# Kernel optimization log

Hardware: AMD Instinct MI355X
Metric: run time of the kernel (lower is better)

The kernel has to match this reference:

```python
import jax, jax.numpy as jnp
import numpy as np

B, C, H, P = 8, 3, 384, 16
DIM, DEPTH, HEADS, MLP = 768, 8, 12, 3072
NP_ = (H // P) ** 2  # 576 patches
PD = C * P * P       # patch_dim = 768
EPS = 1e-5


def _ln(x, g, b):
    m = jnp.mean(x, axis=-1, keepdims=True)
    v = jnp.mean((x - m) ** 2, axis=-1, keepdims=True)
    return (x - m) / jnp.sqrt(v + EPS) * g + b


def setup_inputs() -> dict:
    key = jax.random.key(0)
    ks = jax.random.split(key, 16)
    s = 0.02
    return {
        "img": jax.random.normal(ks[0], (B, C, H, H), jnp.float32),
        "pos_embedding": jax.random.normal(ks[1], (1, NP_ + 1, DIM), jnp.float32),
        "cls_token": jax.random.normal(ks[2], (1, 1, DIM), jnp.float32),
        "patch_w": jax.random.normal(ks[3], (PD, DIM), jnp.float32) * s,
        "patch_b": jnp.zeros((DIM,), jnp.float32),
        "ln1_g": jnp.ones((DEPTH, DIM), jnp.float32),
        "ln1_b": jnp.zeros((DEPTH, DIM), jnp.float32),
        "qkv_w": jax.random.normal(ks[4], (DEPTH, DIM, 3 * DIM), jnp.float32) * s,
        "out_w": jax.random.normal(ks[5], (DEPTH, DIM, DIM), jnp.float32) * s,
        "out_b": jnp.zeros((DEPTH, DIM), jnp.float32),
        "ln2_g": jnp.ones((DEPTH, DIM), jnp.float32),
        "ln2_b": jnp.zeros((DEPTH, DIM), jnp.float32),
        "ff1_w": jax.random.normal(ks[6], (DEPTH, DIM, MLP), jnp.float32) * s,
        "ff1_b": jnp.zeros((DEPTH, MLP), jnp.float32),
        "ff2_w": jax.random.normal(ks[7], (DEPTH, MLP, DIM), jnp.float32) * s,
        "ff2_b": jnp.zeros((DEPTH, DIM), jnp.float32),
    }


def reference(img, pos_embedding, cls_token, patch_w, patch_b,
              ln1_g, ln1_b, qkv_w, out_w, out_b,
              ln2_g, ln2_b, ff1_w, ff1_b, ff2_w, ff2_b):
    b = img.shape[0]
    hp = H // P
    # b c (h p1) (w p2) -> b (h w) (p1 p2 c)
    x = img.reshape(b, C, hp, P, hp, P).transpose(0, 2, 4, 3, 5, 1).reshape(b, hp * hp, P * P * C)
    x = x @ patch_w + patch_b
    x = jnp.concatenate([jnp.broadcast_to(cls_token, (b, 1, DIM)), x], axis=1)
    x = x + pos_embedding[:, : x.shape[1]]

    def layer(xc, p):
        g1, b1, wqkv, wo, bo, g2, b2, w1, bf1, w2, bf2 = p
        y = _ln(xc, g1, b1)
        qkv = y @ wqkv
        q, k, v = jnp.split(qkv, 3, axis=-1)
        sp = lambda a: a.reshape(b, -1, HEADS, DIM // HEADS).transpose(0, 2, 1, 3)
        q, k, v = sp(q), sp(k), sp(v)
        # NOTE: original code never applies the 1/sqrt(d) scale -- faithful.
        dots = jnp.einsum('bhid,bhjd->bhij', q, k)
        attn = jax.nn.softmax(dots, axis=-1)
        o = jnp.einsum('bhij,bhjd->bhid', attn, v).transpose(0, 2, 1, 3).reshape(b, -1, DIM)
        xc = xc + (o @ wo + bo)
        y = _ln(xc, g2, b2)
        xc = xc + (jax.nn.gelu(y @ w1 + bf1, approximate=False) @ w2 + bf2)
        return xc, None

    x, _ = jax.lax.scan(layer, x, (ln1_g, ln1_b, qkv_w, out_w, out_b,
                                   ln2_g, ln2_b, ff1_w, ff1_b, ff2_w, ff2_b))
    return x[:, 1:, :]
```

## Files before the change

kernel.cpp:

```cpp
#include <hip/hip_runtime.h>
#include <hip/hip_bf16.h>
#include <math.h>

#define BB 8
#define CC 3
#define HH 384
#define PP 16
#define HP 24
#define NP 576
#define PD 768
#define DIM 768
#define DEPTH 8
#define HEADS 12
#define DH 64
#define MLP 3072
#define SS 577
#define BS (BB*SS)
#define MPAD 4736
#define LN_EPS 1e-5f
#define NKT 10
#define QW (3*DIM)

typedef __attribute__((ext_vector_type(8))) short s8v;
typedef __attribute__((ext_vector_type(4))) float f4v;

__device__ __forceinline__ float bf2f(unsigned short s) {
    union { unsigned u; float f; } x;
    x.u = ((unsigned)s) << 16;
    return x.f;
}
__device__ __forceinline__ unsigned short f2bfu(float f) {
    __hip_bfloat16 h = __float2bfloat16(f);
    return *reinterpret_cast<unsigned short*>(&h);
}

__device__ __forceinline__ void async16(void* lds, const void* g) {
    __builtin_amdgcn_global_load_lds(
        (const __attribute__((address_space(1))) void*)(uintptr_t)g,
        (__attribute__((address_space(3))) void*)(unsigned)(uintptr_t)lds,
        16, 0, 0);
}

__global__ __launch_bounds__(256) void patchify_k(const float* __restrict__ img,
                                                  unsigned short* __restrict__ xp) {
    int idx = blockIdx.x * 256 + threadIdx.x;
    const int total = BB * NP * PD;
    if (idx >= total) return;
    int b = idx / (NP * PD);
    int r = idx % (NP * PD);
    int n = r / PD;
    int j = r % PD;
    int c  = j % CC;
    int t  = j / CC;
    int p2 = t % PP;
    int p1 = t / PP;
    int hh = n / HP;
    int ww = n % HP;
    int row = hh * PP + p1;
    int col = ww * PP + p2;
    xp[idx] = f2bfu(img[(((size_t)b * CC + c) * HH + row) * HH + col]);
}

__global__ __launch_bounds__(256) void convT_k(const float* __restrict__ W,
                                               unsigned short* __restrict__ Wt,
                                               int K, int N) {
    __shared__ float t[32][33];
    int tx = threadIdx.x & 31, ty = threadIdx.x >> 5;
    int n0 = blockIdx.x * 32, k0 = blockIdx.y * 32;
#pragma unroll
    for (int i = 0; i < 32; i += 8)
        t[ty + i][tx] = W[(size_t)(k0 + ty + i) * N + n0 + tx];
    __syncthreads();
#pragma unroll
    for (int i = 0; i < 32; i += 8)
        Wt[(size_t)(n0 + ty + i) * K + k0 + tx] = f2bfu(t[tx][ty + i]);
}

__global__ __launch_bounds__(256) void convT4_k(const float* __restrict__ s0,
                                                const float* __restrict__ s1,
                                                const float* __restrict__ s2,
                                                const float* __restrict__ s3,
                                                unsigned short* __restrict__ d0,
                                                unsigned short* __restrict__ d1,
                                                unsigned short* __restrict__ d2,
                                                unsigned short* __restrict__ d3) {
    __shared__ float t[32][33];
    int bid = blockIdx.x;
    const float* S; unsigned short* D; int K, N, lt;
    if (bid < 1728)      { S = s0; D = d0; K = 768;  N = 2304; lt = bid; }
    else if (bid < 2304) { S = s1; D = d1; K = 768;  N = 768;  lt = bid - 1728; }
    else if (bid < 4608) { S = s2; D = d2; K = 768;  N = 3072; lt = bid - 2304; }
    else                 { S = s3; D = d3; K = 3072; N = 768;  lt = bid - 4608; }
    int ntn = N >> 5;
    int n0 = (lt % ntn) * 32, k0 = (lt / ntn) * 32;
    int tx = threadIdx.x & 31, ty = threadIdx.x >> 5;
#pragma unroll
    for (int i = 0; i < 32; i += 8)
        t[ty + i][tx] = S[(size_t)(k0 + ty + i) * N + n0 + tx];
    __syncthreads();
#pragma unroll
    for (int i = 0; i < 32; i += 8)
        D[(size_t)(n0 + ty + i) * K + k0 + tx] = f2bfu(t[tx][ty + i]);
}

__global__ __launch_bounds__(256) void build_x_k(const float* __restrict__ pe,
                                                 const float* __restrict__ cls,
                                                 const float* __restrict__ pos,
                                                 float* __restrict__ x) {
    int idx = blockIdx.x * 256 + threadIdx.x;
    const int total = BB * SS * DIM;
    if (idx >= total) return;
    int b = idx / (SS * DIM);
    int r = idx % (SS * DIM);
    int i = r / DIM;
    int d = r % DIM;
    float p = pos[i * DIM + d];
    float v = (i == 0) ? cls[d] : pe[((size_t)b * NP + (i - 1)) * DIM + d];
    x[idx] = v + p;
}

template <int NPART>
__global__ __launch_bounds__(256) void ln_k(const float* __restrict__ x,
                                            const float* __restrict__ P,
                                            const float* __restrict__ g,
                                            const float* __restrict__ bt,
                                            unsigned short* __restrict__ y,
                                            float* __restrict__ xout) {
    __shared__ float sm[8];
    int row = blockIdx.x, tid = threadIdx.x;
    const float* xr = x + (size_t)row * DIM;
    float v0 = xr[tid], v1 = xr[tid + 256], v2 = xr[tid + 512];
    if (NPART == 2) {
        const float* p0 = P + (size_t)row * DIM;
        const float* p1 = P + (size_t)(BS + row) * DIM;
        v0 += p0[tid]       + p1[tid];
        v1 += p0[tid + 256] + p1[tid + 256];
        v2 += p0[tid + 512] + p1[tid + 512];
        float* xo = xout + (size_t)row * DIM;
        xo[tid] = v0; xo[tid + 256] = v1; xo[tid + 512] = v2;
    }
    float s = v0 + v1 + v2;
    for (int o = 32; o; o >>= 1) s += __shfl_xor(s, o);
    if ((tid & 63) == 0) sm[tid >> 6] = s;
    __syncthreads();
    float mean = (sm[0] + sm[1] + sm[2] + sm[3]) * (1.f / 768.f);
    float q0 = v0 - mean, q1 = v1 - mean, q2 = v2 - mean;
    float s2 = q0 * q0 + q1 * q1 + q2 * q2;
    for (int o = 32; o; o >>= 1) s2 += __shfl_xor(s2, o);
    if ((tid & 63) == 0) sm[4 + (tid >> 6)] = s2;
    __syncthreads();
    float var = (sm[4] + sm[5] + sm[6] + sm[7]) * (1.f / 768.f);
    float rstd = rsqrtf(var + LN_EPS);
    unsigned short* yr = y + (size_t)row * DIM;
    yr[tid]       = f2bfu(q0 * rstd * g[tid]       + bt[tid]);
    yr[tid + 256] = f2bfu(q1 * rstd * g[tid + 256] + bt[tid + 256]);
    yr[tid + 512] = f2bfu(q2 * rstd * g[tid + 512] + bt[tid + 512]);
}

template <int OP, int SPLIT>
__global__ __launch_bounds__(256) void mgemm_k(const unsigned short* __restrict__ A,
                                               const unsigned short* __restrict__ Bt,
                                               const float* __restrict__ bias,
                                               void* __restrict__ Cv,
                                               int M, int N, int K) {
    __shared__ unsigned short Al[2][128 * 32];
    __shared__ unsigned short Bl[2][128 * 32];
    int tid = threadIdx.x;
    int wv = tid >> 6, lane = tid & 63;
    int quad = lane >> 4, l16 = lane & 15;
    int m0 = blockIdx.y * 128, n0 = blockIdx.x * 128;
    int wm = (wv >> 1) * 64, wn = (wv & 1) * 64;
    int rg = lane >> 2;
    int kc = (lane & 3) * 8;

    const int Ks = K / SPLIT;
    const int kbase = blockIdx.z * Ks;
    const int T = Ks / 32;

    f4v acc[4][4];
    const f4v zero = {0.f, 0.f, 0.f, 0.f};
#pragma unroll
    for (int i = 0; i < 4; ++i)
#pragma unroll
        for (int j = 0; j < 4; ++j) acc[i][j] = zero;

    auto stage = [&](int t, int bufi) {
#pragma unroll
        for (int gg = 0; gg < 2; ++gg) {
            int g = wv + gg * 4;
            const unsigned short* ga =
                A + (size_t)(m0 + g * 16 + rg) * K + kbase + t * 32 + kc;
            async16(&Al[bufi][g * 512], ga);
            const unsigned short* gb =
                Bt + (size_t)(n0 + g * 16 + rg) * K + kbase + t * 32 + kc;
            async16(&Bl[bufi][g * 512], gb);
        }
    };

    stage(0, 0);
    __syncthreads();

    for (int t = 0; t < T; ++t) {
        int cur = t & 1;
        if (t + 1 < T) stage(t + 1, cur ^ 1);

        s8v af[4], bfr[4];
#pragma unroll
        for (int i = 0; i < 4; ++i)
            af[i] = *reinterpret_cast<const s8v*>(&Al[cur][(wm + i * 16 + l16) * 32 + quad * 8]);
#pragma unroll
        for (int j = 0; j < 4; ++j)
            bfr[j] = *reinterpret_cast<const s8v*>(&Bl[cur][(wn + j * 16 + l16) * 32 + quad * 8]);
#pragma unroll
        for (int i = 0; i < 4; ++i)
#pragma unroll
            for (int j = 0; j < 4; ++j)
                acc[i][j] = __builtin_amdgcn_mfma_f32_16x16x32_bf16(af[i], bfr[j], acc[i][j], 0, 0, 0);

        if (t + 1 < T) __syncthreads();
    }

#pragma unroll
    for (int j = 0; j < 4; ++j) {
        int col = n0 + wn + j * 16 + l16;
        float bj = bias ? bias[col] : 0.f;
        if (SPLIT > 1 && blockIdx.z != 0) bj = 0.f;
#pragma unroll
        for (int i = 0; i < 4; ++i) {
#pragma unroll
            for (int r = 0; r < 4; ++r) {
                int row = m0 + wm + i * 16 + quad * 4 + r;
                if (row >= M) continue;
                float v = acc[i][j][r] + bj;
                size_t idx = (size_t)row * N + col;
                if (OP == 0) {
                    ((unsigned short*)Cv)[idx] = f2bfu(v);
                } else if (OP == 1) {
                    v = 0.5f * v * (1.f + erff(v * 0.70710678118654752f));
                    ((unsigned short*)Cv)[idx] = f2bfu(v);
                } else if (OP == 2) {
                    float* C = (float*)Cv;
                    if (SPLIT > 1) atomicAdd(&C[idx], v);
                    else C[idx] += v;
                } else if (OP == 3) {
                    ((float*)Cv)[idx] = v;
                } else {
                    float* C = (float*)Cv + (size_t)blockIdx.z * ((size_t)M * N);
                    C[idx] = v;
                }
            }
        }
    }
}

__global__ __launch_bounds__(256) void mattn_k(const unsigned short* __restrict__ qkv,
                                               unsigned short* __restrict__ o) {
    __shared__ unsigned short Kl[64 * 72];
    __shared__ unsigned short Vt[64 * 72];
    __shared__ unsigned short Pw[4][16 * 72];

    int tid = threadIdx.x;
    int w = tid >> 6, lane = tid & 63, quad = lane >> 4, l16 = lane & 15;
    int bh = blockIdx.x;
    int b = bh / HEADS, h = bh % HEADS;
    int q0 = blockIdx.y * 64;

    int qq = q0 + w * 16 + l16;
    if (qq > SS - 1) qq = SS - 1;
    const unsigned short* qp = qkv + (size_t)(b * SS + qq) * QW + h * DH + quad * 8;
    s8v aq0 = *reinterpret_cast<const s8v*>(qp);
    s8v aq1 = *reinterpret_cast<const s8v*>(qp + 32);

    float m[4], l[4];
    f4v O[4];
    const f4v zero = {0.f, 0.f, 0.f, 0.f};
#pragma unroll
    for (int r = 0; r < 4; ++r) { m[r] = -INFINITY; l[r] = 0.f; }
#pragma unroll
    for (int dg = 0; dg < 4; ++dg) O[dg] = zero;

    for (int t = 0; t < NKT; ++t) {
        int k0 = t * 64;
        __syncthreads();
#pragma unroll
        for (int rr = 0; rr < 2; ++rr) {
            int cid = tid + rr * 256;
            int row = cid >> 3, cb = (cid & 7) * 8;
            s8v kv = *reinterpret_cast<const s8v*>(
                qkv + (size_t)(b * SS + k0 + row) * QW + DIM + h * DH + cb);
            *reinterpret_cast<s8v*>(&Kl[row * 72 + cb]) = kv;
        }
        {
            int kb = (tid & 15) * 4, db = (tid >> 4) * 4;
            const unsigned short* vb = qkv + (size_t)(b * SS + k0 + kb) * QW + 2 * DIM + h * DH + db;
            ushort4 r0 = *reinterpret_cast<const ushort4*>(vb);
            ushort4 r1 = *reinterpret_cast<const ushort4*>(vb + QW);
            ushort4 r2 = *reinterpret_cast<const ushort4*>(vb + 2 * QW);
            ushort4 r3 = *reinterpret_cast<const ushort4*>(vb + 3 * QW);
            ushort4 w0 = {r0.x, r1.x, r2.x, r3.x};
            ushort4 w1 = {r0.y, r1.y, r2.y, r3.y};
            ushort4 w2 = {r0.z, r1.z, r2.z, r3.z};
            ushort4 w3 = {r0.w, r1.w, r2.w, r3.w};
            *reinterpret_cast<ushort4*>(&Vt[(db + 0) * 72 + kb]) = w0;
            *reinterpret_cast<ushort4*>(&Vt[(db + 1) * 72 + kb]) = w1;
            *reinterpret_cast<ushort4*>(&Vt[(db + 2) * 72 + kb]) = w2;
            *reinterpret_cast<ushort4*>(&Vt[(db + 3) * 72 + kb]) = w3;
        }
        __syncthreads();

        f4v s[4];
#pragma unroll
        for (int kk = 0; kk < 4; ++kk) {
            const unsigned short* kp = &Kl[(kk * 16 + l16) * 72 + quad * 8];
            s8v b0 = *reinterpret_cast<const s8v*>(kp);
            s8v b1 = *reinterpret_cast<const s8v*>(kp + 32);
            f4v z = zero;
            z = __builtin_amdgcn_mfma_f32_16x16x32_bf16(aq0, b0, z, 0, 0, 0);
            z = __builtin_amdgcn_mfma_f32_16x16x32_bf16(aq1, b1, z, 0, 0, 0);
            s[kk] = z;
        }
        int kvalid = SS - k0;
        if (kvalid < 64) {
#pragma unroll
            for (int kk = 0; kk < 4; ++kk)
                if (kk * 16 + l16 >= kvalid) {
                    f4v mk = {-1e30f, -1e30f, -1e30f, -1e30f};
                    s[kk] = mk;
                }
        }
        float alpha[4];
#pragma unroll
        for (int r = 0; r < 4; ++r) {
            float mx = fmaxf(fmaxf(s[0][r], s[1][r]), fmaxf(s[2][r], s[3][r]));
#pragma unroll
            for (int off = 1; off < 16; off <<= 1) mx = fmaxf(mx, __shfl_xor(mx, off));
            float mn = fmaxf(m[r], mx);
            alpha[r] = __expf(m[r] - mn);
            m[r] = mn;
            float ps = 0.f;
#pragma unroll
            for (int kk = 0; kk < 4; ++kk) {
                float p = __expf(s[kk][r] - mn);
                ps += p;
                Pw[w][(quad * 4 + r) * 72 + kk * 16 + l16] = f2bfu(p);
            }
#pragma unroll
            for (int off = 1; off < 16; off <<= 1) ps += __shfl_xor(ps, off);
            l[r] = l[r] * alpha[r] + ps;
        }
#pragma unroll
        for (int dg = 0; dg < 4; ++dg)
#pragma unroll
            for (int r = 0; r < 4; ++r) O[dg][r] *= alpha[r];

        s8v ap0 = *reinterpret_cast<const s8v*>(&Pw[w][l16 * 72 + quad * 8]);
        s8v ap1 = *reinterpret_cast<const s8v*>(&Pw[w][l16 * 72 + 32 + quad * 8]);
#pragma unroll
        for (int dg = 0; dg < 4; ++dg) {
            const unsigned short* vp = &Vt[(dg * 16 + l16) * 72 + quad * 8];
            s8v bv0 = *reinterpret_cast<const s8v*>(vp);
            s8v bv1 = *reinterpret_cast<const s8v*>(vp + 32);
            O[dg] = __builtin_amdgcn_mfma_f32_16x16x32_bf16(ap0, bv0, O[dg], 0, 0, 0);
            O[dg] = __builtin_amdgcn_mfma_f32_16x16x32_bf16(ap1, bv1, O[dg], 0, 0, 0);
        }
    }

#pragma unroll
    for (int r = 0; r < 4; ++r) {
        int q = q0 + w * 16 + quad * 4 + r;
        if (q >= SS) continue;
        float inv = 1.f / l[r];
        unsigned short* op = o + (size_t)(b * SS + q) * DIM + h * DH + l16;
#pragma unroll
        for (int dg = 0; dg < 4; ++dg)
            op[dg * 16] = f2bfu(O[dg][r] * inv);
    }
}

template <int NPART>
__global__ __launch_bounds__(256) void copy_out_k(const float* __restrict__ x,
                                                  const float* __restrict__ P,
                                                  float* __restrict__ out) {
    int idx = blockIdx.x * 256 + threadIdx.x;
    const int total = BB * NP * DIM;
    if (idx >= total) return;
    int b = idx / (NP * DIM);
    int r = idx % (NP * DIM);
    int n = r / DIM;
    int d = r % DIM;
    size_t row = (size_t)b * SS + 1 + n;
    float v = x[row * DIM + d];
    if (NPART == 2)
        v += P[row * DIM + d] + P[(size_t)BS * DIM + row * DIM + d];
    out[idx] = v;
}

extern "C" void kernel_launch(void* const* d_in, const int* in_sizes, int n_in,
                              void* d_out, int out_size, void* d_ws, size_t ws_size,
                              hipStream_t stream) {
    const float* img     = (const float*)d_in[0];
    const float* pos     = (const float*)d_in[1];
    const float* cls     = (const float*)d_in[2];
    const float* patch_w = (const float*)d_in[3];
    const float* patch_b = (const float*)d_in[4];
    const float* ln1_g   = (const float*)d_in[5];
    const float* ln1_b   = (const float*)d_in[6];
    const float* qkv_w   = (const float*)d_in[7];
    const float* out_w   = (const float*)d_in[8];
    const float* out_b   = (const float*)d_in[9];
    const float* ln2_g   = (const float*)d_in[10];
    const float* ln2_b   = (const float*)d_in[11];
    const float* ff1_w   = (const float*)d_in[12];
    const float* ff1_b   = (const float*)d_in[13];
    const float* ff2_w   = (const float*)d_in[14];
    const float* ff2_b   = (const float*)d_in[15];
    float* out = (float*)d_out;

    char* base = (char*)d_ws;
    float* x = (float*)base;                          base += (size_t)BS * DIM * 4;
    unsigned short* y_bf   = (unsigned short*)base;   base += (size_t)MPAD * DIM * 2;
    unsigned short* t1_bf  = (unsigned short*)base;   base += (size_t)MPAD * DIM * 2;
    unsigned short* qkv_bf = (unsigned short*)base;   base += (size_t)MPAD * 3 * DIM * 2;
    unsigned short* hid_bf = (unsigned short*)base;   base += (size_t)MPAD * MLP * 2;
    unsigned short* xp_bf  = (unsigned short*)base;   base += (size_t)BB * NP * PD * 2;
    unsigned short* wq_t = (unsigned short*)base;     base += (size_t)(3 * DIM) * DIM * 2;
    unsigned short* wo_t = (unsigned short*)base;     base += (size_t)DIM * DIM * 2;
    unsigned short* w1_t = (unsigned short*)base;     base += (size_t)MLP * DIM * 2;
    unsigned short* w2_t = (unsigned short*)base;     base += (size_t)DIM * MLP * 2;
    float* part = (float*)base;                       base += (size_t)2 * BS * DIM * 4;
    float* pe_f32 = (float*)hid_bf;

    const int threads = 256;
    const int mblk = (BS + 127) / 128;

    patchify_k<<<(BB * NP * PD + 255) / 256, threads, 0, stream>>>(img, xp_bf);
    convT_k<<<dim3(DIM / 32, PD / 32), threads, 0, stream>>>(patch_w, wq_t, PD, DIM);
    mgemm_k<3, 1><<<dim3(DIM / 128, (BB * NP) / 128), threads, 0, stream>>>(
        xp_bf, wq_t, patch_b, pe_f32, BB * NP, DIM, PD);
    build_x_k<<<(BB * SS * DIM + 255) / 256, threads, 0, stream>>>(pe_f32, cls, pos, x);

    for (int l = 0; l < DEPTH; ++l) {
        if (l == 0)
            ln_k<0><<<BS, threads, 0, stream>>>(x, nullptr, ln1_g, ln1_b, y_bf, nullptr);
        else
            ln_k<2><<<BS, threads, 0, stream>>>(x, part, ln1_g + l * DIM, ln1_b + l * DIM,
                                                y_bf, x);
        convT4_k<<<6912, threads, 0, stream>>>(
            qkv_w + (size_t)l * DIM * 3 * DIM,
            out_w + (size_t)l * DIM * DIM,
            ff1_w + (size_t)l * DIM * MLP,
            ff2_w + (size_t)l * MLP * DIM,
            wq_t, wo_t, w1_t, w2_t);
        mgemm_k<0, 1><<<dim3(3 * DIM / 128, mblk), threads, 0, stream>>>(
            y_bf, wq_t, nullptr, qkv_bf, BS, 3 * DIM, DIM);
        mattn_k<<<dim3(BB * HEADS, NKT), threads, 0, stream>>>(qkv_bf, t1_bf);
        mgemm_k<4, 2><<<dim3(DIM / 128, mblk, 2), threads, 0, stream>>>(
            t1_bf, wo_t, out_b + l * DIM, part, BS, DIM, DIM);
        ln_k<2><<<BS, threads, 0, stream>>>(x, part, ln2_g + l * DIM, ln2_b + l * DIM,
                                            y_bf, x);
        mgemm_k<1, 1><<<dim3(MLP / 128, mblk), threads, 0, stream>>>(
            y_bf, w1_t, ff1_b + l * MLP, hid_bf, BS, MLP, DIM);
        mgemm_k<4, 2><<<dim3(DIM / 128, mblk, 2), threads, 0, stream>>>(
            hid_bf, w2_t, ff2_b + l * DIM, part, BS, DIM, MLP);
    }

    copy_out_k<2><<<(BB * NP * DIM + 255) / 256, threads, 0, stream>>>(x, part, out);
}
```

Baseline: 2.019 ms.

## Triple-buffer GEMM LDS staging with XOR swizzle and setprio around MFMA

Moves the bf16 MFMA GEMM from double to triple LDS buffering. Loads are issued two tiles ahead and gated with explicit vmcnt waits plus a single barrier per iteration, so global-load latency can overlap compute. It also XOR-swizzles the 16-byte k-chunk position on both the async store and the fragment read to reduce LDS bank conflicts, and raises wave priority during the MFMA block. This costs more LDS per block, which may lower occupancy, and the hand-counted vmcnt(4) ties correctness to the number of loads per stage.

```diff
diff --git a/kernel.cpp b/kernel.cpp
--- a/kernel.cpp
+++ b/kernel.cpp
@@ -163,15 +163,16 @@
                                                const float* __restrict__ bias,
                                                void* __restrict__ Cv,
                                                int M, int N, int K) {
-    __shared__ unsigned short Al[2][128 * 32];
-    __shared__ unsigned short Bl[2][128 * 32];
+    __shared__ unsigned short Al[3][128 * 32];
+    __shared__ unsigned short Bl[3][128 * 32];
     int tid = threadIdx.x;
     int wv = tid >> 6, lane = tid & 63;
     int quad = lane >> 4, l16 = lane & 15;
     int m0 = blockIdx.y * 128, n0 = blockIdx.x * 128;
     int wm = (wv >> 1) * 64, wn = (wv & 1) * 64;
     int rg = lane >> 2;
-    int kc = (lane & 3) * 8;
+    int kc = (((lane & 3) ^ (rg & 3)) * 8);
+    int rslot = ((quad ^ (l16 & 3)) * 8);
 
     const int Ks = K / SPLIT;
     const int kbase = blockIdx.z * Ks;
@@ -197,28 +198,40 @@
         }
     };
 
-    stage(0, 0);
-    __syncthreads();
-
-    for (int t = 0; t < T; ++t) {
-        int cur = t & 1;
-        if (t + 1 < T) stage(t + 1, cur ^ 1);
-
+    auto compute = [&](int cur) {
         s8v af[4], bfr[4];
 #pragma unroll
         for (int i = 0; i < 4; ++i)
-            af[i] = *reinterpret_cast<const s8v*>(&Al[cur][(wm + i * 16 + l16) * 32 + quad * 8]);
+            af[i] = *reinterpret_cast<const s8v*>(&Al[cur][(wm + i * 16 + l16) * 32 + rslot]);
 #pragma unroll
         for (int j = 0; j < 4; ++j)
-            bfr[j] = *reinterpret_cast<const s8v*>(&Bl[cur][(wn + j * 16 + l16) * 32 + quad * 8]);
+            bfr[j] = *reinterpret_cast<const s8v*>(&Bl[cur][(wn + j * 16 + l16) * 32 + rslot]);
+        __builtin_amdgcn_s_setprio(1);
 #pragma unroll
         for (int i = 0; i < 4; ++i)
 #pragma unroll
             for (int j = 0; j < 4; ++j)
                 acc[i][j] = __builtin_amdgcn_mfma_f32_16x16x32_bf16(af[i], bfr[j], acc[i][j], 0, 0, 0);
-
-        if (t + 1 < T) __syncthreads();
-    }
+        __builtin_amdgcn_s_setprio(0);
+    };
+
+    stage(0, 0);
+    stage(1, 1);
+
+    int cur = 0, pre = 2;
+    for (int t = 0; t < T - 1; ++t) {
+        asm volatile("s_waitcnt vmcnt(4)" ::: "memory");
+        __builtin_amdgcn_s_barrier();
+        asm volatile("" ::: "memory");
+        if (t + 2 < T) stage(t + 2, pre);
+        compute(cur);
+        cur = (cur == 2) ? 0 : cur + 1;
+        pre = (pre == 2) ? 0 : pre + 1;
+    }
+    asm volatile("s_waitcnt vmcnt(0)" ::: "memory");
+    __builtin_amdgcn_s_barrier();
+    asm volatile("" ::: "memory");
+    compute(cur);
 
 #pragma unroll
     for (int j = 0; j < 4; ++j) {
```

New measurement: 1.997 ms. About the same (-1.1%).

## Restructure GEMM with 8 waves, intra-block K split, swizzled LDS, deeper prefetch

Applied to the files above, without the earlier changes.

The bf16 MFMA GEMM now runs 512 threads per block. Pairs of waves split each 64-wide K tile and their partial accumulators are merged through LDS at the end. LDS tiles grow to K=64 with an XOR swizzle to avoid bank conflicts. Loads are prefetched two tiles ahead using explicit vmcnt waits, raw barriers and s_setprio around the MFMA block. The aim is to hide global-load latency and raise MFMA utilisation, at the cost of more LDS use, an extra reduction step and lower occupancy per block.

```diff
diff --git a/kernel.cpp b/kernel.cpp
--- a/kernel.cpp
+++ b/kernel.cpp
@@ -158,24 +158,25 @@
 }
 
 template <int OP, int SPLIT>
-__global__ __launch_bounds__(256) void mgemm_k(const unsigned short* __restrict__ A,
+__global__ __launch_bounds__(512) void mgemm_k(const unsigned short* __restrict__ A,
                                                const unsigned short* __restrict__ Bt,
                                                const float* __restrict__ bias,
                                                void* __restrict__ Cv,
                                                int M, int N, int K) {
-    __shared__ unsigned short Al[2][128 * 32];
-    __shared__ unsigned short Bl[2][128 * 32];
+    __shared__ unsigned short Lds[2][2][128 * 64];
     int tid = threadIdx.x;
     int wv = tid >> 6, lane = tid & 63;
     int quad = lane >> 4, l16 = lane & 15;
+    int kp = wv & 1;
+    int pos = wv >> 1;
+    int wm = (pos >> 1) * 64, wn = (pos & 1) * 64;
     int m0 = blockIdx.y * 128, n0 = blockIdx.x * 128;
-    int wm = (wv >> 1) * 64, wn = (wv & 1) * 64;
-    int rg = lane >> 2;
-    int kc = (lane & 3) * 8;
+    int srow = lane >> 3;
+    int sk = ((lane & 7) ^ srow) * 8;
 
     const int Ks = K / SPLIT;
     const int kbase = blockIdx.z * Ks;
-    const int T = Ks / 32;
+    const int T = Ks / 64;
 
     f4v acc[4][4];
     const f4v zero = {0.f, 0.f, 0.f, 0.f};
@@ -186,39 +187,69 @@
 
     auto stage = [&](int t, int bufi) {
 #pragma unroll
-        for (int gg = 0; gg < 2; ++gg) {
-            int g = wv + gg * 4;
+        for (int s2 = 0; s2 < 2; ++s2) {
+            int sub = wv * 2 + s2;
+            int row = sub * 8 + srow;
             const unsigned short* ga =
-                A + (size_t)(m0 + g * 16 + rg) * K + kbase + t * 32 + kc;
-            async16(&Al[bufi][g * 512], ga);
+                A + (size_t)(m0 + row) * K + kbase + t * 64 + sk;
+            async16(&Lds[bufi][0][sub * 512], ga);
             const unsigned short* gb =
-                Bt + (size_t)(n0 + g * 16 + rg) * K + kbase + t * 32 + kc;
-            async16(&Bl[bufi][g * 512], gb);
+                Bt + (size_t)(n0 + row) * K + kbase + t * 64 + sk;
+            async16(&Lds[bufi][1][sub * 512], gb);
         }
     };
 
     stage(0, 0);
-    __syncthreads();
+    stage(1, 1);
+
+    const int coff = ((kp * 4 + quad) ^ (l16 & 7)) << 3;
 
     for (int t = 0; t < T; ++t) {
         int cur = t & 1;
-        if (t + 1 < T) stage(t + 1, cur ^ 1);
-
-        s8v af[4], bfr[4];
+        if (t < T - 1) asm volatile("s_waitcnt vmcnt(4)" ::: "memory");
+        else           asm volatile("s_waitcnt vmcnt(0)" ::: "memory");
+        __builtin_amdgcn_s_barrier();
+
+        s8v af[4], bf[4];
 #pragma unroll
         for (int i = 0; i < 4; ++i)
-            af[i] = *reinterpret_cast<const s8v*>(&Al[cur][(wm + i * 16 + l16) * 32 + quad * 8]);
+            af[i] = *reinterpret_cast<const s8v*>(
+                &Lds[cur][0][(wm + i * 16 + l16) * 64 + coff]);
 #pragma unroll
         for (int j = 0; j < 4; ++j)
-            bfr[j] = *reinterpret_cast<const s8v*>(&Bl[cur][(wn + j * 16 + l16) * 32 + quad * 8]);
+            bf[j] = *reinterpret_cast<const s8v*>(
+                &Lds[cur][1][(wn + j * 16 + l16) * 64 + coff]);
+        asm volatile("s_waitcnt lgkmcnt(0)" ::: "memory");
+        __builtin_amdgcn_sched_barrier(0);
+        __builtin_amdgcn_s_barrier();
+        if (t + 2 < T) stage(t + 2, cur);
+
+        __builtin_amdgcn_s_setprio(1);
 #pragma unroll
         for (int i = 0; i < 4; ++i)
 #pragma unroll
             for (int j = 0; j < 4; ++j)
-                acc[i][j] = __builtin_amdgcn_mfma_f32_16x16x32_bf16(af[i], bfr[j], acc[i][j], 0, 0, 0);
-
-        if (t + 1 < T) __syncthreads();
-    }
+                acc[i][j] = __builtin_amdgcn_mfma_f32_16x16x32_bf16(af[i], bf[j], acc[i][j], 0, 0, 0);
+        __builtin_amdgcn_s_setprio(0);
+    }
+
+    __builtin_amdgcn_s_barrier();
+    float* mrg = (float*)&Lds[0][0][0];
+    if (kp == 1) {
+#pragma unroll
+        for (int i = 0; i < 4; ++i)
+#pragma unroll
+            for (int j = 0; j < 4; ++j)
+                *reinterpret_cast<f4v*>(&mrg[pos * 4096 + (i * 4 + j) * 256 + lane * 4]) = acc[i][j];
+    }
+    asm volatile("s_waitcnt lgkmcnt(0)" ::: "memory");
+    __builtin_amdgcn_s_barrier();
+    if (kp != 0) return;
+#pragma unroll
+    for (int i = 0; i < 4; ++i)
+#pragma unroll
+        for (int j = 0; j < 4; ++j)
+            acc[i][j] += *reinterpret_cast<const f4v*>(&mrg[pos * 4096 + (i * 4 + j) * 256 + lane * 4]);
 
 #pragma unroll
     for (int j = 0; j < 4; ++j) {
@@ -431,11 +462,12 @@
     float* pe_f32 = (float*)hid_bf;
 
     const int threads = 256;
+    const int gthreads = 512;
     const int mblk = (BS + 127) / 128;
 
     patchify_k<<<(BB * NP * PD + 255) / 256, threads, 0, stream>>>(img, xp_bf);
     convT_k<<<dim3(DIM / 32, PD / 32), threads, 0, stream>>>(patch_w, wq_t, PD, DIM);
-    mgemm_k<3, 1><<<dim3(DIM / 128, (BB * NP) / 128), threads, 0, stream>>>(
+    mgemm_k<3, 1><<<dim3(DIM / 128, (BB * NP) / 128), gthreads, 0, stream>>>(
         xp_bf, wq_t, patch_b, pe_f32, BB * NP, DIM, PD);
     build_x_k<<<(BB * SS * DIM + 255) / 256, threads, 0, stream>>>(pe_f32, cls, pos, x);
 
@@ -451,16 +483,16 @@
             ff1_w + (size_t)l * DIM * MLP,
             ff2_w + (size_t)l * MLP * DIM,
             wq_t, wo_t, w1_t, w2_t);
-        mgemm_k<0, 1><<<dim3(3 * DIM / 128, mblk), threads, 0, stream>>>(
+        mgemm_k<0, 1><<<dim3(3 * DIM / 128, mblk), gthreads, 0, stream>>>(
             y_bf, wq_t, nullptr, qkv_bf, BS, 3 * DIM, DIM);
         mattn_k<<<dim3(BB * HEADS, NKT), threads, 0, stream>>>(qkv_bf, t1_bf);
-        mgemm_k<4, 2><<<dim3(DIM / 128, mblk, 2), threads, 0, stream>>>(
+        mgemm_k<4, 2><<<dim3(DIM / 128, mblk, 2), gthreads, 0, stream>>>(
             t1_bf, wo_t, out_b + l * DIM, part, BS, DIM, DIM);
         ln_k<2><<<BS, threads, 0, stream>>>(x, part, ln2_g + l * DIM, ln2_b + l * DIM,
                                             y_bf, x);
-        mgemm_k<1, 1><<<dim3(MLP / 128, mblk), threads, 0, stream>>>(
+        mgemm_k<1, 1><<<dim3(MLP / 128, mblk), gthreads, 0, stream>>>(
             y_bf, w1_t, ff1_b + l * MLP, hid_bf, BS, MLP, DIM);
-        mgemm_k<4, 2><<<dim3(DIM / 128, mblk, 2), threads, 0, stream>>>(
+        mgemm_k<4, 2><<<dim3(DIM / 128, mblk, 2), gthreads, 0, stream>>>(
             hid_bf, w2_t, ff2_b + l * DIM, part, BS, DIM, MLP);
     }
 
```

Result: slower. 2.444 ms (+21.1%).

## Double GEMM K-tile to 64 with XOR-swizzled LDS and explicit waitcnt barrier

Applied to the files above, without the earlier changes.

Raises the GEMM K-step from 32 to 64 so each iteration issues twice as many MFMAs per barrier, and stores LDS tiles with an XOR swizzle on 16-byte chunks to avoid bank conflicts on fragment reads. The synchronization is restructured into a single vmcnt(0) wait plus s_barrier at the top of each iteration, and s_setprio is raised around the MFMA block. LDS use doubles to 64KB per block, which may reduce occupancy. K must now be divisible by 64 per split.

```diff
diff --git a/kernel.cpp b/kernel.cpp
--- a/kernel.cpp
+++ b/kernel.cpp
@@ -163,19 +163,19 @@
                                                const float* __restrict__ bias,
                                                void* __restrict__ Cv,
                                                int M, int N, int K) {
-    __shared__ unsigned short Al[2][128 * 32];
-    __shared__ unsigned short Bl[2][128 * 32];
+    __shared__ unsigned short Al[2][128 * 64];
+    __shared__ unsigned short Bl[2][128 * 64];
     int tid = threadIdx.x;
     int wv = tid >> 6, lane = tid & 63;
     int quad = lane >> 4, l16 = lane & 15;
     int m0 = blockIdx.y * 128, n0 = blockIdx.x * 128;
     int wm = (wv >> 1) * 64, wn = (wv & 1) * 64;
-    int rg = lane >> 2;
-    int kc = (lane & 3) * 8;
+    int srow = lane >> 3;
+    int schunk = ((lane & 7) ^ srow) * 8;
 
     const int Ks = K / SPLIT;
     const int kbase = blockIdx.z * Ks;
-    const int T = Ks / 32;
+    const int T = Ks / 64;
 
     f4v acc[4][4];
     const f4v zero = {0.f, 0.f, 0.f, 0.f};
@@ -186,38 +186,49 @@
 
     auto stage = [&](int t, int bufi) {
 #pragma unroll
-        for (int gg = 0; gg < 2; ++gg) {
-            int g = wv + gg * 4;
+        for (int s = 0; s < 4; ++s) {
+            int sub = wv * 4 + s;
+            int row = sub * 8 + srow;
             const unsigned short* ga =
-                A + (size_t)(m0 + g * 16 + rg) * K + kbase + t * 32 + kc;
-            async16(&Al[bufi][g * 512], ga);
+                A + (size_t)(m0 + row) * K + kbase + t * 64 + schunk;
+            async16(&Al[bufi][sub * 512], ga);
             const unsigned short* gb =
-                Bt + (size_t)(n0 + g * 16 + rg) * K + kbase + t * 32 + kc;
-            async16(&Bl[bufi][g * 512], gb);
+                Bt + (size_t)(n0 + row) * K + kbase + t * 64 + schunk;
+            async16(&Bl[bufi][sub * 512], gb);
         }
     };
 
     stage(0, 0);
-    __syncthreads();
 
     for (int t = 0; t < T; ++t) {
         int cur = t & 1;
+        asm volatile("s_waitcnt vmcnt(0)" ::: "memory");
+        __builtin_amdgcn_s_barrier();
+        asm volatile("" ::: "memory");
         if (t + 1 < T) stage(t + 1, cur ^ 1);
 
-        s8v af[4], bfr[4];
+        s8v af[2][4], bf[2][4];
+#pragma unroll
+        for (int kc = 0; kc < 2; ++kc) {
+            int slot = ((kc * 4 + quad) ^ (l16 & 7)) * 8;
+#pragma unroll
+            for (int i = 0; i < 4; ++i)
+                af[kc][i] = *reinterpret_cast<const s8v*>(
+                    &Al[cur][(wm + i * 16 + l16) * 64 + slot]);
+#pragma unroll
+            for (int j = 0; j < 4; ++j)
+                bf[kc][j] = *reinterpret_cast<const s8v*>(
+                    &Bl[cur][(wn + j * 16 + l16) * 64 + slot]);
+        }
+        __builtin_amdgcn_s_setprio(1);
 #pragma unroll
         for (int i = 0; i < 4; ++i)
-            af[i] = *reinterpret_cast<const s8v*>(&Al[cur][(wm + i * 16 + l16) * 32 + quad * 8]);
-#pragma unroll
-        for (int j = 0; j < 4; ++j)
-            bfr[j] = *reinterpret_cast<const s8v*>(&Bl[cur][(wn + j * 16 + l16) * 32 + quad * 8]);
-#pragma unroll
-        for (int i = 0; i < 4; ++i)
-#pragma unroll
-            for (int j = 0; j < 4; ++j)
-                acc[i][j] = __builtin_amdgcn_mfma_f32_16x16x32_bf16(af[i], bfr[j], acc[i][j], 0, 0, 0);
-
-        if (t + 1 < T) __syncthreads();
+#pragma unroll
+            for (int j = 0; j < 4; ++j) {
+                acc[i][j] = __builtin_amdgcn_mfma_f32_16x16x32_bf16(af[0][i], bf[0][j], acc[i][j], 0, 0, 0);
+                acc[i][j] = __builtin_amdgcn_mfma_f32_16x16x32_bf16(af[1][i], bf[1][j], acc[i][j], 0, 0, 0);
+            }
+        __builtin_amdgcn_s_setprio(0);
     }
 
 #pragma unroll
```

New measurement: 1.955 ms. 1.03x faster.
